# Kernel tuning notes

Hardware: AMD Instinct MI355X
Metric: run time of the kernel (lower is better)

## Reference

```python
import jax, jax.numpy as jnp
import numpy as np

N_NODES = 100000
N_EDGES = 600000
D = 128
BN_EPS = 1e-5


def setup_inputs() -> dict:
    key = jax.random.key(0)
    k1, k2, k3 = jax.random.split(key, 3)
    x = jax.random.normal(k1, (N_NODES, D), dtype=jnp.float32)
    edge_index = jax.random.randint(k2, (2, N_EDGES), 0, N_NODES, dtype=jnp.int64)
    # Linear(in=D, out=D): kaiming-uniform-ish init
    W = jax.random.normal(k3, (D, D), dtype=jnp.float32) / np.sqrt(D)
    b = jnp.zeros((D,), dtype=jnp.float32)
    eps_gin = jnp.zeros((), dtype=jnp.float32)  # train_eps=True, init 0
    gamma = jnp.ones((D,), dtype=jnp.float32)
    beta = jnp.zeros((D,), dtype=jnp.float32)
    return {"x": x, "edge_index": edge_index, "W": W, "b": b,
            "eps_gin": eps_gin, "gamma": gamma, "beta": beta}


def reference(x, edge_index, W, b, eps_gin, gamma, beta):
    src, dst = edge_index[0], edge_index[1]
    # GIN aggregation: sum of source features into destination nodes
    agg = jax.ops.segment_sum(x[src], dst, num_segments=N_NODES)  # [N, D]
    h = (1.0 + eps_gin) * x + agg
    # MLP([D, D]) == single Linear (PyG plain_last)
    h = jnp.einsum('nd,df->nf', h, W.T) + b  # torch Linear: h @ W^T + b
    # BatchNorm1d in training mode (batch stats, biased variance)
    mean = jnp.mean(h, axis=0)
    var = jnp.mean((h - mean) ** 2, axis=0)
    h = (h - mean) * jax.lax.rsqrt(var + BN_EPS) * gamma + beta
    h = jax.nn.relu(h)
    # residual
    return h + x
```

## Files before the change

### kernel.cpp

```cpp
#include <hip/hip_runtime.h>
#include <hip/hip_bf16.h>

#define N_NODES 100000
#define N_EDGES 600000
#define D 128
#define BN_EPS 1e-5f
#define CAP 32
#define CAST_BLOCKS 6250
#define FILL_BLOCKS ((N_EDGES + 255) / 256)
#define GEMM_GRID 1024
#define NSLOT 32

typedef __bf16 bf16x8 __attribute__((ext_vector_type(8)));
typedef float floatx4 __attribute__((ext_vector_type(4)));
typedef unsigned short ushortx8 __attribute__((ext_vector_type(8)));

__device__ __forceinline__ unsigned short f2bf(float f) {
    union { float f; unsigned u; } v; v.f = f;
    unsigned u = v.u;
    unsigned r = u + 0x7FFFu + ((u >> 16) & 1u);
    return (unsigned short)(r >> 16);
}
__device__ __forceinline__ float bf2f(unsigned short u) {
    union { unsigned u; float f; } v; v.u = ((unsigned)u) << 16;
    return v.f;
}

__global__ __launch_bounds__(256) void k_prep(const float* __restrict__ x,
                                              const int* __restrict__ ei,
                                              int* __restrict__ cursor,
                                              int* __restrict__ bucket,
                                              unsigned short* __restrict__ xb) {
    int b = blockIdx.x;
    if (b < CAST_BLOCKS) {
        int idx = (b * 256 + threadIdx.x) * 8;
        float4 a = *(const float4*)(x + idx);
        float4 c = *(const float4*)(x + idx + 4);
        ushortx8 u;
        u[0] = f2bf(a.x); u[1] = f2bf(a.y); u[2] = f2bf(a.z); u[3] = f2bf(a.w);
        u[4] = f2bf(c.x); u[5] = f2bf(c.y); u[6] = f2bf(c.z); u[7] = f2bf(c.w);
        *(ushortx8*)(xb + idx) = u;
    } else {
        int e = (b - CAST_BLOCKS) * 256 + threadIdx.x;
        if (e >= N_EDGES) return;
        int src = ei[e];
        int dst = ei[N_EDGES + e];
        int pos = atomicAdd(&cursor[dst], 1);
        if (pos < CAP) bucket[dst * CAP + pos] = src;
    }
}

__global__ __launch_bounds__(256) void k_aggregate(const unsigned short* __restrict__ xb,
                                                   const int* __restrict__ cursor,
                                                   const int* __restrict__ bucket,
                                                   const float* __restrict__ epsp,
                                                   unsigned short* __restrict__ h) {
    int tid = blockIdx.x * 256 + threadIdx.x;
    int node = tid >> 4;
    if (node >= N_NODES) return;
    int lane = tid & 15;
    int deg = cursor[node];
    if (deg > CAP) deg = CAP;
    const int* bk = bucket + node * CAP;
    float acc[8] = {0.f, 0.f, 0.f, 0.f, 0.f, 0.f, 0.f, 0.f};
    for (int i = 0; i < deg; ++i) {
        int s = bk[i];
        ushortx8 v = *(const ushortx8*)(xb + (size_t)s * D + lane * 8);
#pragma unroll
        for (int j = 0; j < 8; ++j) acc[j] += bf2f(v[j]);
    }
    const float one_eps = 1.0f + epsp[0];
    ushortx8 xv = *(const ushortx8*)(xb + (size_t)node * D + lane * 8);
    ushortx8 o;
#pragma unroll
    for (int j = 0; j < 8; ++j) o[j] = f2bf(one_eps * bf2f(xv[j]) + acc[j]);
    *(ushortx8*)(h + (size_t)node * D + lane * 8) = o;
}

__device__ __forceinline__ void load_B_frags(const float* __restrict__ W,
                                             int fbase, int n16, int quad,
                                             bf16x8 B[4][4]) {
#pragma unroll
    for (int ft = 0; ft < 4; ++ft) {
#pragma unroll
        for (int ks = 0; ks < 4; ++ks) {
            const float* wp = W + (fbase + ft * 16 + n16) * D + ks * 32 + quad * 8;
            float4 wa = *(const float4*)wp;
            float4 wb = *(const float4*)(wp + 4);
            ushortx8 u;
            u[0] = f2bf(wa.x); u[1] = f2bf(wa.y); u[2] = f2bf(wa.z); u[3] = f2bf(wa.w);
            u[4] = f2bf(wb.x); u[5] = f2bf(wb.y); u[6] = f2bf(wb.z); u[7] = f2bf(wb.w);
            B[ft][ks] = __builtin_bit_cast(bf16x8, u);
        }
    }
}

__global__ __launch_bounds__(256) void k_gemm_stats(const unsigned short* __restrict__ h,
                                                    const float* __restrict__ W,
                                                    float* __restrict__ psums,
                                                    float* __restrict__ psqs) {
    const int lane = threadIdx.x & 63;
    const int wid  = threadIdx.x >> 6;
    const int gw   = blockIdx.x * 4 + wid;
    const int fhalf = gw & 1;
    const int pair  = gw >> 1;
    const int npairs = GEMM_GRID * 2;
    const int n16  = lane & 15;
    const int quad = lane >> 4;
    const int fbase = fhalf * 64;
    const int slot = blockIdx.x & (NSLOT - 1);

    bf16x8 B[4][4];
    load_B_frags(W, fbase, n16, quad, B);

    float psum[4] = {0.f, 0.f, 0.f, 0.f};
    float psq[4]  = {0.f, 0.f, 0.f, 0.f};
    for (int chunk = pair; chunk < N_NODES / 16; chunk += npairs) {
        const int rbase = chunk * 16;
        floatx4 acc[4];
#pragma unroll
        for (int ft = 0; ft < 4; ++ft) acc[ft] = (floatx4){0.f, 0.f, 0.f, 0.f};
#pragma unroll
        for (int ks = 0; ks < 4; ++ks) {
            const unsigned short* hp = h + (size_t)(rbase + n16) * D + ks * 32 + quad * 8;
            bf16x8 a = __builtin_bit_cast(bf16x8, *(const ushortx8*)hp);
#pragma unroll
            for (int ft = 0; ft < 4; ++ft)
                acc[ft] = __builtin_amdgcn_mfma_f32_16x16x32_bf16(a, B[ft][ks], acc[ft], 0, 0, 0);
        }
#pragma unroll
        for (int ft = 0; ft < 4; ++ft) {
#pragma unroll
            for (int i = 0; i < 4; ++i) {
                float v = acc[ft][i];
                psum[ft] += v;
                psq[ft]  += v * v;
            }
        }
    }
#pragma unroll
    for (int ft = 0; ft < 4; ++ft) {
        float s = psum[ft], q = psq[ft];
        s += __shfl_xor(s, 16, 64); q += __shfl_xor(q, 16, 64);
        s += __shfl_xor(s, 32, 64); q += __shfl_xor(q, 32, 64);
        if (quad == 0) {
            int col = fbase + ft * 16 + n16;
            atomicAdd(&psums[slot * D + col], s);
            atomicAdd(&psqs[slot * D + col], q);
        }
    }
}

__global__ __launch_bounds__(256) void k_fin(const unsigned short* __restrict__ h,
                                             const float* __restrict__ W,
                                             const float* __restrict__ x,
                                             const float* __restrict__ psums,
                                             const float* __restrict__ psqs,
                                             const float* __restrict__ gamma,
                                             const float* __restrict__ beta,
                                             float* __restrict__ out) {
    const int lane = threadIdx.x & 63;
    const int wid  = threadIdx.x >> 6;
    const int gw   = blockIdx.x * 4 + wid;
    const int fhalf = gw & 1;
    const int pair  = gw >> 1;
    const int npairs = GEMM_GRID * 2;
    const int n16  = lane & 15;
    const int quad = lane >> 4;
    const int fbase = fhalf * 64;

    bf16x8 B[4][4];
    load_B_frags(W, fbase, n16, quad, B);

    const float inv_n = 1.0f / (float)N_NODES;
    float sc[4], sh[4];
#pragma unroll
    for (int ft = 0; ft < 4; ++ft) {
        int col = fbase + ft * 16 + n16;
        float s = 0.f, q = 0.f;
        for (int k = 0; k < NSLOT; ++k) {
            s += psums[k * D + col];
            q += psqs[k * D + col];
        }
        float mean = s * inv_n;
        float var  = q * inv_n - mean * mean;
        sc[ft] = gamma[col] * rsqrtf(var + BN_EPS);
        sh[ft] = beta[col] - mean * sc[ft];
    }

    for (int chunk = pair; chunk < N_NODES / 16; chunk += npairs) {
        const int rbase = chunk * 16;
        floatx4 acc[4];
#pragma unroll
        for (int ft = 0; ft < 4; ++ft) acc[ft] = (floatx4){0.f, 0.f, 0.f, 0.f};
#pragma unroll
        for (int ks = 0; ks < 4; ++ks) {
            const unsigned short* hp = h + (size_t)(rbase + n16) * D + ks * 32 + quad * 8;
            bf16x8 a = __builtin_bit_cast(bf16x8, *(const ushortx8*)hp);
#pragma unroll
            for (int ft = 0; ft < 4; ++ft)
                acc[ft] = __builtin_amdgcn_mfma_f32_16x16x32_bf16(a, B[ft][ks], acc[ft], 0, 0, 0);
        }
#pragma unroll
        for (int ft = 0; ft < 4; ++ft) {
            const int col = fbase + ft * 16 + n16;
#pragma unroll
            for (int i = 0; i < 4; ++i) {
                size_t off = (size_t)(rbase + quad * 4 + i) * D + col;
                out[off] = fmaxf(acc[ft][i] * sc[ft] + sh[ft], 0.0f) + x[off];
            }
        }
    }
}

extern "C" void kernel_launch(void* const* d_in, const int* in_sizes, int n_in,
                              void* d_out, int out_size, void* d_ws, size_t ws_size,
                              hipStream_t stream) {
    const float* x     = (const float*)d_in[0];
    const int*   ei    = (const int*)d_in[1];
    const float* W     = (const float*)d_in[2];
    const float* epsp  = (const float*)d_in[4];
    const float* gamma = (const float*)d_in[5];
    const float* beta  = (const float*)d_in[6];
    float* out = (float*)d_out;

    char* ws = (char*)d_ws;
    int*   cursor = (int*)ws;
    float* psums  = (float*)(ws + (size_t)N_NODES * 4);
    float* psqs   = psums + NSLOT * D;
    int*   bucket = (int*)((char*)psqs + NSLOT * D * 4);
    unsigned short* xb = (unsigned short*)((char*)bucket + (size_t)N_NODES * CAP * 4);
    unsigned short* h  = xb + (size_t)N_NODES * D;

    hipMemsetAsync(cursor, 0, (size_t)N_NODES * 4 + 2 * NSLOT * D * 4, stream);

    k_prep<<<CAST_BLOCKS + FILL_BLOCKS, 256, 0, stream>>>(x, ei, cursor, bucket, xb);
    k_aggregate<<<(N_NODES * 16 + 255) / 256, 256, 0, stream>>>(xb, cursor, bucket, epsp, h);
    k_gemm_stats<<<GEMM_GRID, 256, 0, stream>>>(h, W, psums, psqs);
    k_fin<<<GEMM_GRID, 256, 0, stream>>>(h, W, x, psums, psqs, gamma, beta, out);
}
```

Measured before the change: 250.4 us.

## Fuse neighbor aggregation into GEMM-stats kernel via LDS tile, read bf16 residual

Merges the gather-sum aggregation and the first GEMM/statistics pass into one persistent kernel. Each block aggregates a 32-node tile into shared memory and runs MFMA on it directly, while still writing h for the final pass. This removes a launch and a global re-read of h. The final kernel now reads the residual from the bf16 copy of x instead of fp32, halving that traffic at some precision cost. Stat slots grow to 64 to spread the atomics, and fewer resident threads may hide gather latency less well.

After: 342.0 us. +36.6%, slower.

```diff
diff --git a/kernel.cpp b/kernel.cpp
--- a/kernel.cpp
+++ b/kernel.cpp
@@ -9,7 +9,10 @@
 #define CAST_BLOCKS 6250
 #define FILL_BLOCKS ((N_EDGES + 255) / 256)
 #define GEMM_GRID 1024
-#define NSLOT 32
+#define NSLOT 64
+#define TILES (N_NODES / 32)
+#define GRID_AG 1568
+#define LDS_STRIDE 136
 
 typedef __bf16 bf16x8 __attribute__((ext_vector_type(8)));
 typedef float floatx4 __attribute__((ext_vector_type(4)));
@@ -32,49 +35,22 @@
                                               int* __restrict__ bucket,
                                               unsigned short* __restrict__ xb) {
     int b = blockIdx.x;
-    if (b < CAST_BLOCKS) {
-        int idx = (b * 256 + threadIdx.x) * 8;
+    if (b < FILL_BLOCKS) {
+        int e = b * 256 + threadIdx.x;
+        if (e >= N_EDGES) return;
+        int src = ei[e];
+        int dst = ei[N_EDGES + e];
+        int pos = atomicAdd(&cursor[dst], 1);
+        if (pos < CAP) bucket[dst * CAP + pos] = src;
+    } else {
+        int idx = ((b - FILL_BLOCKS) * 256 + threadIdx.x) * 8;
         float4 a = *(const float4*)(x + idx);
         float4 c = *(const float4*)(x + idx + 4);
         ushortx8 u;
         u[0] = f2bf(a.x); u[1] = f2bf(a.y); u[2] = f2bf(a.z); u[3] = f2bf(a.w);
         u[4] = f2bf(c.x); u[5] = f2bf(c.y); u[6] = f2bf(c.z); u[7] = f2bf(c.w);
         *(ushortx8*)(xb + idx) = u;
-    } else {
-        int e = (b - CAST_BLOCKS) * 256 + threadIdx.x;
-        if (e >= N_EDGES) return;
-        int src = ei[e];
-        int dst = ei[N_EDGES + e];
-        int pos = atomicAdd(&cursor[dst], 1);
-        if (pos < CAP) bucket[dst * CAP + pos] = src;
-    }
-}
-
-__global__ __launch_bounds__(256) void k_aggregate(const unsigned short* __restrict__ xb,
-                                                   const int* __restrict__ cursor,
-                                                   const int* __restrict__ bucket,
-                                                   const float* __restrict__ epsp,
-                                                   unsigned short* __restrict__ h) {
-    int tid = blockIdx.x * 256 + threadIdx.x;
-    int node = tid >> 4;
-    if (node >= N_NODES) return;
-    int lane = tid & 15;
-    int deg = cursor[node];
-    if (deg > CAP) deg = CAP;
-    const int* bk = bucket + node * CAP;
-    float acc[8] = {0.f, 0.f, 0.f, 0.f, 0.f, 0.f, 0.f, 0.f};
-    for (int i = 0; i < deg; ++i) {
-        int s = bk[i];
-        ushortx8 v = *(const ushortx8*)(xb + (size_t)s * D + lane * 8);
-#pragma unroll
-        for (int j = 0; j < 8; ++j) acc[j] += bf2f(v[j]);
-    }
-    const float one_eps = 1.0f + epsp[0];
-    ushortx8 xv = *(const ushortx8*)(xb + (size_t)node * D + lane * 8);
-    ushortx8 o;
-#pragma unroll
-    for (int j = 0; j < 8; ++j) o[j] = f2bf(one_eps * bf2f(xv[j]) + acc[j]);
-    *(ushortx8*)(h + (size_t)node * D + lane * 8) = o;
+    }
 }
 
 __device__ __forceinline__ void load_B_frags(const float* __restrict__ W,
@@ -95,49 +71,83 @@
     }
 }
 
-__global__ __launch_bounds__(256) void k_gemm_stats(const unsigned short* __restrict__ h,
-                                                    const float* __restrict__ W,
-                                                    float* __restrict__ psums,
-                                                    float* __restrict__ psqs) {
-    const int lane = threadIdx.x & 63;
-    const int wid  = threadIdx.x >> 6;
-    const int gw   = blockIdx.x * 4 + wid;
-    const int fhalf = gw & 1;
-    const int pair  = gw >> 1;
-    const int npairs = GEMM_GRID * 2;
+__global__ __launch_bounds__(256) void k_agg_gemm(const unsigned short* __restrict__ xb,
+                                                  const int* __restrict__ cursor,
+                                                  const int* __restrict__ bucket,
+                                                  const float* __restrict__ epsp,
+                                                  const float* __restrict__ W,
+                                                  unsigned short* __restrict__ h,
+                                                  float* __restrict__ psums,
+                                                  float* __restrict__ psqs) {
+    __shared__ unsigned short tile[32 * LDS_STRIDE];
+
+    const int t    = threadIdx.x;
+    const int wid  = t >> 6;
+    const int lane = t & 63;
     const int n16  = lane & 15;
     const int quad = lane >> 4;
-    const int fbase = fhalf * 64;
-    const int slot = blockIdx.x & (NSLOT - 1);
+    const int ch   = wid & 1;
+    const int fh   = wid >> 1;
+    const int fbase = fh * 64;
+    const int grow  = t >> 4;
+    const int glane = t & 15;
 
     bf16x8 B[4][4];
     load_B_frags(W, fbase, n16, quad, B);
 
+    const float one_eps = 1.0f + epsp[0];
     float psum[4] = {0.f, 0.f, 0.f, 0.f};
     float psq[4]  = {0.f, 0.f, 0.f, 0.f};
-    for (int chunk = pair; chunk < N_NODES / 16; chunk += npairs) {
-        const int rbase = chunk * 16;
-        floatx4 acc[4];
-#pragma unroll
-        for (int ft = 0; ft < 4; ++ft) acc[ft] = (floatx4){0.f, 0.f, 0.f, 0.f};
+
+    for (int tl = blockIdx.x; tl < TILES; tl += GRID_AG) {
+        const int nbase = tl * 32;
+#pragma unroll
+        for (int g = 0; g < 2; ++g) {
+            int row  = g * 16 + grow;
+            int node = nbase + row;
+            int deg = cursor[node];
+            if (deg > CAP) deg = CAP;
+            const int* bk = bucket + node * CAP;
+            float acc[8] = {0.f, 0.f, 0.f, 0.f, 0.f, 0.f, 0.f, 0.f};
+            for (int i = 0; i < deg; ++i) {
+                int s = bk[i];
+                ushortx8 v = *(const ushortx8*)(xb + (size_t)s * D + glane * 8);
+#pragma unroll
+                for (int j = 0; j < 8; ++j) acc[j] += bf2f(v[j]);
+            }
+            ushortx8 xv = *(const ushortx8*)(xb + (size_t)node * D + glane * 8);
+            ushortx8 o;
+#pragma unroll
+            for (int j = 0; j < 8; ++j) o[j] = f2bf(one_eps * bf2f(xv[j]) + acc[j]);
+            *(ushortx8*)(h + (size_t)node * D + glane * 8) = o;
+            *(ushortx8*)(tile + row * LDS_STRIDE + glane * 8) = o;
+        }
+        __syncthreads();
+
+        floatx4 acc4[4];
+#pragma unroll
+        for (int ft = 0; ft < 4; ++ft) acc4[ft] = (floatx4){0.f, 0.f, 0.f, 0.f};
 #pragma unroll
         for (int ks = 0; ks < 4; ++ks) {
-            const unsigned short* hp = h + (size_t)(rbase + n16) * D + ks * 32 + quad * 8;
-            bf16x8 a = __builtin_bit_cast(bf16x8, *(const ushortx8*)hp);
+            const unsigned short* tp = tile + (ch * 16 + n16) * LDS_STRIDE + ks * 32 + quad * 8;
+            bf16x8 a = __builtin_bit_cast(bf16x8, *(const ushortx8*)tp);
 #pragma unroll
             for (int ft = 0; ft < 4; ++ft)
-                acc[ft] = __builtin_amdgcn_mfma_f32_16x16x32_bf16(a, B[ft][ks], acc[ft], 0, 0, 0);
+                acc4[ft] = __builtin_amdgcn_mfma_f32_16x16x32_bf16(a, B[ft][ks], acc4[ft], 0, 0, 0);
         }
 #pragma unroll
         for (int ft = 0; ft < 4; ++ft) {
 #pragma unroll
             for (int i = 0; i < 4; ++i) {
-                float v = acc[ft][i];
+                float v = acc4[ft][i];
                 psum[ft] += v;
                 psq[ft]  += v * v;
             }
         }
-    }
+        __syncthreads();
+    }
+
+    const int slot = (blockIdx.x * 4 + wid) & (NSLOT - 1);
 #pragma unroll
     for (int ft = 0; ft < 4; ++ft) {
         float s = psum[ft], q = psq[ft];
@@ -153,7 +163,7 @@
 
 __global__ __launch_bounds__(256) void k_fin(const unsigned short* __restrict__ h,
                                              const float* __restrict__ W,
-                                             const float* __restrict__ x,
+                                             const unsigned short* __restrict__ xb,
                                              const float* __restrict__ psums,
                                              const float* __restrict__ psqs,
                                              const float* __restrict__ gamma,
@@ -207,7 +217,7 @@
 #pragma unroll
             for (int i = 0; i < 4; ++i) {
                 size_t off = (size_t)(rbase + quad * 4 + i) * D + col;
-                out[off] = fmaxf(acc[ft][i] * sc[ft] + sh[ft], 0.0f) + x[off];
+                out[off] = fmaxf(acc[ft][i] * sc[ft] + sh[ft], 0.0f) + bf2f(xb[off]);
             }
         }
     }
@@ -235,7 +245,6 @@
     hipMemsetAsync(cursor, 0, (size_t)N_NODES * 4 + 2 * NSLOT * D * 4, stream);
 
     k_prep<<<CAST_BLOCKS + FILL_BLOCKS, 256, 0, stream>>>(x, ei, cursor, bucket, xb);
-    k_aggregate<<<(N_NODES * 16 + 255) / 256, 256, 0, stream>>>(xb, cursor, bucket, epsp, h);
-    k_gemm_stats<<<GEMM_GRID, 256, 0, stream>>>(h, W, psums, psqs);
-    k_fin<<<GEMM_GRID, 256, 0, stream>>>(h, W, x, psums, psqs, gamma, beta, out);
-}
+    k_agg_gemm<<<GRID_AG, 256, 0, stream>>>(xb, cursor, bucket, epsp, W, h, psums, psqs);
+    k_fin<<<GEMM_GRID, 256, 0, stream>>>(h, W, xb, psums, psqs, gamma, beta, out);
+}
```
